# Optimization experiments

Measured on AMD Instinct MI355X. Metric: run time of the kernel, lower is better.

The kernel has to match this reference:

```python
import jax, jax.numpy as jnp
import numpy as np

N = 65536          # points in cloud
K = 10             # neighbor_count
P = 25             # kernel points (shells 1+8+16)
CIN = 1
COUT = 64
SIGMA = 2.1 * 0.05 # kernel radius used as influence extent
CELL = 0.05 * 2    # grid_max_pool cell size
GRID = 10          # points in [0,1)^3 -> 10 bins per axis
NSEG = GRID ** 3
CHUNK = 2048       # kNN query chunk


def setup_inputs() -> dict:
    key = jax.random.key(0)
    k1, k2, k3 = jax.random.split(key, 3)
    points1 = jax.random.uniform(k1, (N, 3), dtype=jnp.float32)
    kernel = jax.random.normal(k2, (P, 3), dtype=jnp.float32) * 0.05  # kernel point dispositions within radius
    W = jax.random.normal(k3, (P, CIN, COUT), dtype=jnp.float32) * 0.1
    return {"points1": points1, "kernel": kernel, "W": W}


def _knn_indices(query, support, k):
    # chunked brute-force kNN; never materializes the full NxN distance matrix
    sn = jnp.sum(support * support, axis=-1)  # [N]
    def chunk_knn(q):  # q: [CHUNK,3]
        d = jnp.sum(q * q, axis=-1)[:, None] - 2.0 * (q @ support.T) + sn[None, :]
        return jax.lax.top_k(-d, k)[1]  # [CHUNK,K]
    idx = jax.lax.map(chunk_knn, query.reshape(-1, CHUNK, 3))
    return idx.reshape(query.shape[0], k)


def _kpconv(query, support, features, kernel, W, k, sigma):
    idx = _knn_indices(query, support, k)          # [N,K] int32
    nfeat = features[idx]                          # [N,K,Cin] gather
    rel = support[idx] - query[:, None, :]         # [N,K,3] relative neighbor positions
    diff = rel[:, :, None, :] - kernel[None, None, :, :]   # [N,K,P,3]
    dist = jnp.sqrt(jnp.sum(diff * diff, axis=-1))         # [N,K,P]
    infl = jnp.maximum(0.0, 1.0 - dist / sigma)            # linear kernel-point influence
    weighted = jnp.einsum('nkp,nkc->npc', infl, nfeat)     # [N,P,Cin]
    return jnp.einsum('npc,pcd->nd', weighted, W)          # [N,Cout]


def _grid_mean_pool(points, features, cell):
    gid = jnp.floor(points / cell).astype(jnp.int32)       # [N,3] voxel coords in [0,GRID)
    seg = (gid[:, 0] * GRID + gid[:, 1]) * GRID + gid[:, 2]
    ones = jnp.ones((points.shape[0],), points.dtype)
    counts = jax.ops.segment_sum(ones, seg, num_segments=NSEG)   # [NSEG]
    denom = jnp.maximum(counts, 1.0)[:, None]
    points_sub = jax.ops.segment_sum(points, seg, num_segments=NSEG) / denom    # per-voxel mean of points
    feats_sub = jax.ops.segment_sum(features, seg, num_segments=NSEG) / denom   # per-voxel mean of features
    return points_sub, feats_sub


def reference(points1, kernel, W):
    ones_feat = jnp.ones((points1.shape[0], CIN), points1.dtype)
    features2 = _kpconv(points1, points1, ones_feat, kernel, W, K, SIGMA)
    points3, features3 = _grid_mean_pool(points1, features2, CELL)
    return points3, features3
```

## Files before the change

### kernel.cpp

```cpp
#include <hip/hip_runtime.h>
#include <math.h>

#define NPTS  65536
#define KNN   10
#define PK    25
#define NCOUT 64
#define GRIDB 10
#define NSEG  1000
#define GRIDC 20
#define NCELL 8000
#define CELLK 0.05f
#define R0SQ  0.002025f
#define SLAB_CAP 832
#define LIST_CAP 48
#define LIST_STRIDE 49
#define INVSIG (1.0f / (2.1f * 0.05f))

#define OFF_SORTED  0
#define OFF_HIST    1048576
#define OFF_UCNT    1080576
#define OFF_CSTART  1080580
#define OFF_CURSOR  1112584
#define OFF_ULST    1144584
#define OFF_KNN     1406736
#define MEMSET_SIZE 32004

__device__ __forceinline__ int cell_of(float px, float py, float pz) {
    int gx = min((int)(px * (float)GRIDC), GRIDC - 1);
    int gy = min((int)(py * (float)GRIDC), GRIDC - 1);
    int gz = min((int)(pz * (float)GRIDC), GRIDC - 1);
    return (gx * GRIDC + gy) * GRIDC + gz;
}

__global__ __launch_bounds__(256) void hist_kernel(
    const float* __restrict__ pts, int* __restrict__ hist)
{
    int g = blockIdx.x * 256 + threadIdx.x;
    float px = pts[g*3+0], py = pts[g*3+1], pz = pts[g*3+2];
    atomicAdd(&hist[cell_of(px, py, pz)], 1);
}

__global__ __launch_bounds__(256) void scan_kernel(
    const int* __restrict__ hist, int* __restrict__ cstart, int* __restrict__ cursor)
{
    __shared__ int part[256];
    const int t = threadIdx.x;
    const int base = t * 32;
    int s = 0;
    for (int i = 0; i < 32; ++i) {
        int c = base + i;
        s += (c < NCELL) ? hist[c] : 0;
    }
    part[t] = s;
    __syncthreads();
    for (int off = 1; off < 256; off <<= 1) {
        int v = (t >= off) ? part[t - off] : 0;
        __syncthreads();
        part[t] += v;
        __syncthreads();
    }
    int run = (t == 0) ? 0 : part[t - 1];
    for (int i = 0; i < 32; ++i) {
        int c = base + i;
        if (c < NCELL) {
            cstart[c] = run;
            cursor[c] = run;
            run += hist[c];
        }
    }
    if (t == 255) cstart[NCELL] = run;
}

__global__ __launch_bounds__(256) void scatter_kernel(
    const float* __restrict__ pts, int* __restrict__ cursor, float4* __restrict__ sorted)
{
    int g = blockIdx.x * 256 + threadIdx.x;
    float px = pts[g*3+0], py = pts[g*3+1], pz = pts[g*3+2];
    int c = cell_of(px, py, pz);
    int pos = atomicAdd(&cursor[c], 1);
    sorted[pos] = make_float4(px, py, pz, 0.f);
}

__device__ __forceinline__ void insert10(float (&kd)[KNN], int (&ki)[KNN],
                                         float d, int idx)
{
    float cd = d; int ci = idx;
#pragma unroll
    for (int u = 0; u < KNN; ++u) {
        bool lt = cd < kd[u];
        float td = kd[u]; int ti = ki[u];
        kd[u] = lt ? cd : kd[u];
        ki[u] = lt ? ci : ki[u];
        cd = lt ? td : cd;
        ci = lt ? ti : ci;
    }
}

__device__ __forceinline__ void ins10_64(unsigned long long (&kd)[KNN],
                                         unsigned long long v) {
#pragma unroll
    for (int u = 0; u < KNN; ++u) {
        bool lt = v < kd[u];
        unsigned long long lo = lt ? v : kd[u];
        unsigned long long hi = lt ? kd[u] : v;
        kd[u] = lo; v = hi;
    }
}

__global__ __launch_bounds__(64) void knn_kernel(
    const float4* __restrict__ sorted,
    const int*    __restrict__ cstart,
    unsigned short* __restrict__ knn,
    int*          __restrict__ ucnt,
    int*          __restrict__ ulst)
{
    __shared__ float4 cand[SLAB_CAP];
    __shared__ unsigned short gidx[SLAB_CAP];
    __shared__ unsigned short lst[64 * LIST_STRIDE];

    const int tid = threadIdx.x;
    const int col = blockIdx.x / 3;
    const int seg = blockIdx.x % 3;
    const int cx = col / GRIDC, cy = col % GRIDC;
    const int cz0 = (seg < 2) ? seg * 7 : 14;
    const int len = (seg < 2) ? 7 : 6;
    const int colBase = col * GRIDC;

    const int qb = cstart[colBase + cz0];
    const int qe = cstart[colBase + cz0 + len];
    const int qn = qe - qb;
    if (qn == 0) return;

    const int zA = max(cz0 - 1, 0);
    const int zB = min(cz0 + len, GRIDC - 1);

    int cB4 = 0, cS4 = 0;
    int ncand = 0;
    {
        int cB[9], cS[9], cL[9];
#pragma unroll
        for (int a = 0; a < 3; ++a)
#pragma unroll
            for (int b = 0; b < 3; ++b) {
                int c = a * 3 + b;
                int xx = cx - 1 + a, yy = cy - 1 + b;
                bool v = ((unsigned)xx < GRIDC) && ((unsigned)yy < GRIDC);
                int cc = v ? (xx * GRIDC + yy) * GRIDC : 0;
                int s0 = v ? cstart[cc + zA] : 0;
                int e0 = v ? cstart[cc + zB + 1] : 0;
                cS[c] = s0; cB[c] = ncand; cL[c] = e0 - s0;
                ncand += e0 - s0;
            }
        cB4 = cB[4]; cS4 = cS[4];
#pragma unroll
        for (int c = 0; c < 9; ++c) {
            int lim = min(cL[c], max(0, SLAB_CAP - cB[c]));
            for (int i = tid; i < lim; i += 64) {
                float4 p = sorted[cS[c] + i];
                gidx[cB[c] + i] = (unsigned short)(cS[c] + i);
                p.w = p.x*p.x + p.y*p.y + p.z*p.z;
                cand[cB[c] + i] = p;
            }
        }
    }
    const bool slabOvf = (ncand > SLAB_CAP);
    const int nscan = min(ncand, SLAB_CAP);
    __syncthreads();

    const int lb = tid * LIST_STRIDE;

    for (int qbase = 0; qbase < qn; qbase += 64) {
        const bool active = (qbase + tid) < qn;
        const int qidx = qb + qbase + (active ? tid : 0);

        if (slabOvf) {
            if (active) ulst[atomicAdd(ucnt, 1)] = qidx;
            continue;
        }

        const float4 Q = cand[cB4 + (qidx - cS4)];
        const float qq = Q.w;
        const float m2x = -2.f*Q.x, m2y = -2.f*Q.y, m2z = -2.f*Q.z;

        int cnt = 0;
#pragma unroll 4
        for (int j = 0; j < nscan; ++j) {
            float4 s = cand[j];
            float t = fmaf(m2x, s.x, s.w);
            t = fmaf(m2y, s.y, t);
            t = fmaf(m2z, s.z, t);
            float d = t + qq;
            lst[lb + min(cnt, LIST_CAP)] = (unsigned short)j;
            cnt += (d < R0SQ) ? 1 : 0;
        }

        const bool resolved = active && (cnt >= KNN) && (cnt <= LIST_CAP);
        if (active && !resolved) ulst[atomicAdd(ucnt, 1)] = qidx;

        if (resolved) {
            float kd[KNN]; int ki[KNN];
#pragma unroll
            for (int u = 0; u < KNN; ++u) { kd[u] = 3.4e38f; ki[u] = 0; }
            for (int i = 0; i < cnt; ++i) {
                int j = lst[lb + i];
                float4 s = cand[j];
                float t = fmaf(m2x, s.x, s.w);
                t = fmaf(m2y, s.y, t);
                t = fmaf(m2z, s.z, t);
                float d = t + qq;
                if (d < kd[KNN-1]) insert10(kd, ki, d, j);
            }
#pragma unroll
            for (int u = 0; u < KNN; ++u)
                knn[qidx * 16 + u] = gidx[ki[u]];
        }
    }
}

__global__ __launch_bounds__(64) void phaseB(
    const float4* __restrict__ sorted,
    const int*    __restrict__ cstart,
    unsigned short* __restrict__ knn,
    const int*    __restrict__ ucnt,
    const int*    __restrict__ ulst)
{
    const int lane = threadIdx.x;
    const int n = *ucnt;

    for (int w = blockIdx.x; w < n; w += gridDim.x) {
        const int qidx = ulst[w];
        const float4 Q = sorted[qidx];
        const int cqx = min((int)(Q.x * (float)GRIDC), GRIDC - 1);
        const int cqy = min((int)(Q.y * (float)GRIDC), GRIDC - 1);
        const int cqz = min((int)(Q.z * (float)GRIDC), GRIDC - 1);

        int r = 2;
        while (true) {
            unsigned long long kd[KNN];
#pragma unroll
            for (int u = 0; u < KNN; ++u) kd[u] = ~0ull;
            const int x0 = max(cqx-r,0), x1 = min(cqx+r,GRIDC-1);
            const int y0 = max(cqy-r,0), y1 = min(cqy+r,GRIDC-1);
            const int z0 = max(cqz-r,0), z1 = min(cqz+r,GRIDC-1);
            for (int xx = x0; xx <= x1; ++xx)
                for (int yy = y0; yy <= y1; ++yy) {
                    const int cc = (xx * GRIDC + yy) * GRIDC;
                    const int b0 = cstart[cc + z0], e0 = cstart[cc + z1 + 1];
                    for (int i = b0 + lane; i < e0; i += 64) {
                        float4 s = sorted[i];
                        float dx = Q.x - s.x, dy = Q.y - s.y, dz = Q.z - s.z;
                        float d = dx * dx;
                        d = fmaf(dy, dy, d);
                        d = fmaf(dz, dz, d);
                        unsigned long long pk =
                            ((unsigned long long)__float_as_uint(d) << 32) | (unsigned)i;
                        if (pk < kd[KNN-1]) ins10_64(kd, pk);
                    }
                }
            float d10 = 0.f;
#pragma unroll
            for (int t = 0; t < KNN; ++t) {
                unsigned long long m = kd[0];
#pragma unroll
                for (int off = 1; off < 64; off <<= 1) {
                    unsigned long long o = __shfl_xor(m, off);
                    m = (o < m) ? o : m;
                }
                if (lane == 0) knn[qidx * 16 + t] = (unsigned short)(unsigned)m;
                d10 = __uint_as_float((unsigned)(m >> 32));
                bool win = (kd[0] == m);
#pragma unroll
                for (int u = 0; u < KNN-1; ++u) kd[u] = win ? kd[u+1] : kd[u];
                kd[KNN-1] = win ? ~0ull : kd[KNN-1];
            }
            float rr = r * CELLK;
            if (d10 <= rr * rr || r >= GRIDC) break;
            ++r;
        }
    }
}

__global__ __launch_bounds__(64) void gather_pool(
    const float4* __restrict__ sorted,
    const int*    __restrict__ cstart,
    const unsigned short* __restrict__ knn,
    const float*  __restrict__ kern,
    const float*  __restrict__ W,
    float*        __restrict__ out)
{
    __shared__ float kx[PK], ky[PK], kz[PK];
    const int lane = threadIdx.x;
    const int s = blockIdx.x;
    const int Z = s % GRIDB, Y = (s / GRIDB) % GRIDB, X = s / (GRIDB * GRIDB);

    if (lane < PK) { kx[lane]=kern[lane*3]; ky[lane]=kern[lane*3+1]; kz[lane]=kern[lane*3+2]; }
    __syncthreads();

    int rb[4], rl[4];
#pragma unroll
    for (int a = 0; a < 2; ++a)
#pragma unroll
        for (int b = 0; b < 2; ++b) {
            int cc = ((2*X + a) * GRIDC + (2*Y + b)) * GRIDC + 2*Z;
            int b0 = cstart[cc], e0 = cstart[cc + 2];
            rb[a*2+b] = b0; rl[a*2+b] = e0 - b0;
        }
    const int c0 = rl[0], c1 = c0 + rl[1], c2 = c1 + rl[2];
    const int qn = c2 + rl[3];

    float acc[PK];
#pragma unroll
    for (int p = 0; p < PK; ++p) acc[p] = 0.f;
    float cntL = 0.f, sxL = 0.f, syL = 0.f, szL = 0.f;

    for (int base = 0; base < qn; base += 64) {
        int i = base + lane;
        if (i < qn) {
            int qidx;
            if (i < c0)      qidx = rb[0] + i;
            else if (i < c1) qidx = rb[1] + (i - c0);
            else if (i < c2) qidx = rb[2] + (i - c1);
            else             qidx = rb[3] + (i - c2);

            float4 Q = sorted[qidx];
            const unsigned short* kr = knn + qidx * 16;
            int4 v  = *reinterpret_cast<const int4*>(kr);
            int  v2 = *reinterpret_cast<const int*>(kr + 8);

#pragma unroll
            for (int u = 0; u < KNN; ++u) {
                int w32 = (u < 2) ? v.x : (u < 4) ? v.y : (u < 6) ? v.z
                        : (u < 8) ? v.w : v2;
                int idx = (u & 1) ? ((w32 >> 16) & 0xFFFF) : (w32 & 0xFFFF);
                float4 nb = sorted[idx];
                float rx = nb.x - Q.x, ry = nb.y - Q.y, rz = nb.z - Q.z;
#pragma unroll
                for (int p = 0; p < PK; ++p) {
                    float dx = rx - kx[p], dy = ry - ky[p], dz = rz - kz[p];
                    float d2 = dx * dx;
                    d2 = fmaf(dy, dy, d2);
                    d2 = fmaf(dz, dz, d2);
                    acc[p] += fmaxf(0.f, fmaf(-INVSIG, sqrtf(d2), 1.f));
                }
            }
            cntL += 1.f; sxL += Q.x; syL += Q.y; szL += Q.z;
        }
    }

#pragma unroll
    for (int off = 1; off < 64; off <<= 1) {
        cntL += __shfl_xor(cntL, off);
        sxL  += __shfl_xor(sxL, off);
        syL  += __shfl_xor(syL, off);
        szL  += __shfl_xor(szL, off);
#pragma unroll
        for (int p = 0; p < PK; ++p) acc[p] += __shfl_xor(acc[p], off);
    }

    const float inv = 1.0f / fmaxf(cntL, 1.0f);
    float dotv = 0.f;
#pragma unroll
    for (int p = 0; p < PK; ++p) dotv = fmaf(acc[p], W[p * NCOUT + lane], dotv);
    out[NSEG*3 + s*NCOUT + lane] = dotv * inv;
    if (lane == 0) {
        out[s*3+0] = sxL * inv;
        out[s*3+1] = syL * inv;
        out[s*3+2] = szL * inv;
    }
}

extern "C" void kernel_launch(void* const* d_in, const int* in_sizes, int n_in,
                              void* d_out, int out_size, void* d_ws, size_t ws_size,
                              hipStream_t stream)
{
    const float* pts  = (const float*)d_in[0];
    const float* kern = (const float*)d_in[1];
    const float* W    = (const float*)d_in[2];
    float* out = (float*)d_out;
    char*  ws  = (char*)d_ws;

    float4* sorted = (float4*)(ws + OFF_SORTED);
    int*    hist   = (int*)   (ws + OFF_HIST);
    int*    ucnt   = (int*)   (ws + OFF_UCNT);
    int*    cstart = (int*)   (ws + OFF_CSTART);
    int*    cursor = (int*)   (ws + OFF_CURSOR);
    int*    ulst   = (int*)   (ws + OFF_ULST);
    unsigned short* knn = (unsigned short*)(ws + OFF_KNN);

    hipMemsetAsync(hist, 0, MEMSET_SIZE, stream);

    hist_kernel   <<<NPTS/256, 256, 0, stream>>>(pts, hist);
    scan_kernel   <<<1,        256, 0, stream>>>(hist, cstart, cursor);
    scatter_kernel<<<NPTS/256, 256, 0, stream>>>(pts, cursor, sorted);
    knn_kernel    <<<400*3,     64, 0, stream>>>(sorted, cstart, knn, ucnt, ulst);
    phaseB        <<<4096,      64, 0, stream>>>(sorted, cstart, knn, ucnt, ulst);
    gather_pool   <<<NSEG,      64, 0, stream>>>(sorted, cstart, knn, kern, W, out);
}
```

Baseline: 221.5 us.

## Split kNN candidate scan across four wavefronts per block and merge in wave zero

Result: slower. 320.3 us (+44.6%).

```diff
diff --git a/kernel.cpp b/kernel.cpp
--- a/kernel.cpp
+++ b/kernel.cpp
@@ -12,8 +12,8 @@
 #define CELLK 0.05f
 #define R0SQ  0.002025f
 #define SLAB_CAP 832
-#define LIST_CAP 48
-#define LIST_STRIDE 49
+#define QCAP  16
+#define LSTR  17
 #define INVSIG (1.0f / (2.1f * 0.05f))
 
 #define OFF_SORTED  0
@@ -107,7 +107,7 @@
     }
 }
 
-__global__ __launch_bounds__(64) void knn_kernel(
+__global__ __launch_bounds__(256) void knn_kernel(
     const float4* __restrict__ sorted,
     const int*    __restrict__ cstart,
     unsigned short* __restrict__ knn,
@@ -116,9 +116,12 @@
 {
     __shared__ float4 cand[SLAB_CAP];
     __shared__ unsigned short gidx[SLAB_CAP];
-    __shared__ unsigned short lst[64 * LIST_STRIDE];
-
-    const int tid = threadIdx.x;
+    __shared__ unsigned short lst[256 * LSTR];
+    __shared__ unsigned char  cntS[256];
+
+    const int tid  = threadIdx.x;
+    const int wv   = tid >> 6;
+    const int lane = tid & 63;
     const int col = blockIdx.x / 3;
     const int seg = blockIdx.x % 3;
     const int cx = col / GRIDC, cy = col % GRIDC;
@@ -155,7 +158,7 @@
 #pragma unroll
         for (int c = 0; c < 9; ++c) {
             int lim = min(cL[c], max(0, SLAB_CAP - cB[c]));
-            for (int i = tid; i < lim; i += 64) {
+            for (int i = tid; i < lim; i += 256) {
                 float4 p = sorted[cS[c] + i];
                 gidx[cB[c] + i] = (unsigned short)(cS[c] + i);
                 p.w = p.x*p.x + p.y*p.y + p.z*p.z;
@@ -167,14 +170,16 @@
     const int nscan = min(ncand, SLAB_CAP);
     __syncthreads();
 
-    const int lb = tid * LIST_STRIDE;
+    const int sw = (nscan * wv) >> 2;
+    const int ew = (nscan * (wv + 1)) >> 2;
+    const int lb = tid * LSTR;
 
     for (int qbase = 0; qbase < qn; qbase += 64) {
-        const bool active = (qbase + tid) < qn;
-        const int qidx = qb + qbase + (active ? tid : 0);
+        const bool active = (qbase + lane) < qn;
+        const int qidx = qb + qbase + (active ? lane : 0);
 
         if (slabOvf) {
-            if (active) ulst[atomicAdd(ucnt, 1)] = qidx;
+            if (active && wv == 0) ulst[atomicAdd(ucnt, 1)] = qidx;
             continue;
         }
 
@@ -184,36 +189,50 @@
 
         int cnt = 0;
 #pragma unroll 4
-        for (int j = 0; j < nscan; ++j) {
+        for (int j = sw; j < ew; ++j) {
             float4 s = cand[j];
             float t = fmaf(m2x, s.x, s.w);
             t = fmaf(m2y, s.y, t);
             t = fmaf(m2z, s.z, t);
             float d = t + qq;
-            lst[lb + min(cnt, LIST_CAP)] = (unsigned short)j;
+            lst[lb + min(cnt, QCAP - 1)] = (unsigned short)j;
             cnt += (d < R0SQ) ? 1 : 0;
         }
-
-        const bool resolved = active && (cnt >= KNN) && (cnt <= LIST_CAP);
-        if (active && !resolved) ulst[atomicAdd(ucnt, 1)] = qidx;
-
-        if (resolved) {
-            float kd[KNN]; int ki[KNN];
-#pragma unroll
-            for (int u = 0; u < KNN; ++u) { kd[u] = 3.4e38f; ki[u] = 0; }
-            for (int i = 0; i < cnt; ++i) {
-                int j = lst[lb + i];
-                float4 s = cand[j];
-                float t = fmaf(m2x, s.x, s.w);
-                t = fmaf(m2y, s.y, t);
-                t = fmaf(m2z, s.z, t);
-                float d = t + qq;
-                if (d < kd[KNN-1]) insert10(kd, ki, d, j);
+        cntS[tid] = (unsigned char)min(cnt, 255);
+        __syncthreads();
+
+        if (wv == 0) {
+            int c0 = cntS[lane], c1 = cntS[64 + lane],
+                c2 = cntS[128 + lane], c3 = cntS[192 + lane];
+            int total = c0 + c1 + c2 + c3;
+            bool ok = active && total >= KNN &&
+                      c0 <= QCAP && c1 <= QCAP && c2 <= QCAP && c3 <= QCAP;
+            if (active && !ok) ulst[atomicAdd(ucnt, 1)] = qidx;
+
+            if (ok) {
+                float kd[KNN]; int ki[KNN];
+#pragma unroll
+                for (int u = 0; u < KNN; ++u) { kd[u] = 3.4e38f; ki[u] = 0; }
+#pragma unroll
+                for (int w = 0; w < 4; ++w) {
+                    int cw = (w == 0) ? c0 : (w == 1) ? c1 : (w == 2) ? c2 : c3;
+                    int wb = (w * 64 + lane) * LSTR;
+                    for (int i = 0; i < cw; ++i) {
+                        int j = lst[wb + i];
+                        float4 s = cand[j];
+                        float t = fmaf(m2x, s.x, s.w);
+                        t = fmaf(m2y, s.y, t);
+                        t = fmaf(m2z, s.z, t);
+                        float d = t + qq;
+                        if (d < kd[KNN-1]) insert10(kd, ki, d, j);
+                    }
+                }
+#pragma unroll
+                for (int u = 0; u < KNN; ++u)
+                    knn[qidx * 16 + u] = gidx[ki[u]];
             }
-#pragma unroll
-            for (int u = 0; u < KNN; ++u)
-                knn[qidx * 16 + u] = gidx[ki[u]];
-        }
+        }
+        __syncthreads();
     }
 }
 
@@ -392,7 +411,7 @@
     hist_kernel   <<<NPTS/256, 256, 0, stream>>>(pts, hist);
     scan_kernel   <<<1,        256, 0, stream>>>(hist, cstart, cursor);
     scatter_kernel<<<NPTS/256, 256, 0, stream>>>(pts, cursor, sorted);
-    knn_kernel    <<<400*3,     64, 0, stream>>>(sorted, cstart, knn, ucnt, ulst);
-    phaseB        <<<4096,      64, 0, stream>>>(sorted, cstart, knn, ucnt, ulst);
+    knn_kernel    <<<400*3,    256, 0, stream>>>(sorted, cstart, knn, ucnt, ulst);
+    phaseB        <<<2048,      64, 0, stream>>>(sorted, cstart, knn, ucnt, ulst);
     gather_pool   <<<NSEG,      64, 0, stream>>>(sorted, cstart, knn, kern, W, out);
 }
```
